# Kernel tuning notes

Measured on AMD Instinct MI355X. Metric: run time of the kernel, lower is better.

## Reference

```python
import jax, jax.numpy as jnp
import numpy as np

BITS = 4
MASK = (1 << BITS) - 1  # 15
PACK = 32 // BITS       # 8 values per int32


def setup_inputs() -> dict:
    key = jax.random.key(0)
    k1, k2, k3, k4, k5 = jax.random.split(key, 5)
    K, N, T = 4096, 4096, 8192
    x = jax.random.normal(k1, (T, K), dtype=jnp.float32)
    qweight = jax.random.randint(k2, (K * BITS // 32, N), 0, 2**31 - 1, dtype=jnp.int32)
    qzeros = jax.random.randint(k3, (1, N * BITS // 32), 0, 2**31 - 1, dtype=jnp.int32)
    scales = jax.random.uniform(k4, (1, N), dtype=jnp.float32) * 0.01
    g_idx = jnp.zeros((K,), dtype=jnp.int32)  # single group (group_size == infeatures)
    bias = jax.random.normal(k5, (N,), dtype=jnp.float32)
    return {"x": x, "qweight": qweight, "qzeros": qzeros, "scales": scales,
            "g_idx": g_idx, "bias": bias}


def reference(x, qweight, qzeros, scales, g_idx, bias):
    shifts = jnp.arange(0, 32, BITS, dtype=jnp.int32)  # (8,)
    # Unpack weights: (K/8, N) int32 -> (K/8, 8, N) -> (K, N) ints in [0, 15]
    w_int = (qweight[:, None, :] >> shifts[None, :, None]) & MASK
    K = w_int.shape[0] * PACK
    w_int = w_int.reshape(K, -1)
    # Unpack zero-points: (G, N/8) int32 -> (G, N/8, 8) -> (G, N), +1 per GPTQ convention
    z_int = ((qzeros[:, :, None] >> shifts[None, None, :]) & MASK) + 1
    z_int = z_int.reshape(scales.shape)  # (G, N)
    # Dequantize per input row via group index gather
    g = g_idx.astype(jnp.int32)
    w = scales[g] * (w_int.astype(scales.dtype) - z_int[g].astype(scales.dtype))  # (K, N)
    out = jnp.matmul(x, w) + bias  # (T, N)
    return out
```

## Files before the change

### kernel.cpp

```cpp
#include <hip/hip_runtime.h>
#include <stdint.h>

#define T_DIM 8192
#define K_DIM 4096
#define N_DIM 4096

typedef __attribute__((ext_vector_type(8))) short bf16x8;
typedef __attribute__((ext_vector_type(8))) unsigned short u16x8;
typedef __attribute__((ext_vector_type(4))) float f32x4;

__device__ __forceinline__ unsigned short f2bf(float f) {
  union { float f; uint32_t u; } c; c.f = f;
  uint32_t u = c.u;
  uint32_t r = (u + 0x7fffu + ((u >> 16) & 1u)) >> 16;
  return (unsigned short)r;
}
__device__ __forceinline__ float bf2f(unsigned short b) {
  union { uint32_t u; float f; } c; c.u = ((uint32_t)b) << 16;
  return c.f;
}

__global__ void unpack_bt(const int* __restrict__ qweight, const int* __restrict__ qzeros,
                          unsigned short* __restrict__ bt) {
  const int t  = threadIdx.x;
  const int n  = blockIdx.y * 32 + (t >> 3);
  const int kk = blockIdx.x * 8 + (t & 7);
  const int qw = qweight[(size_t)kk * N_DIM + n];
  const int zw = qzeros[n >> 3];
  const int z  = ((zw >> ((n & 7) * 4)) & 15) + 1;
  u16x8 v;
#pragma unroll
  for (int i = 0; i < 8; ++i) {
    const int w = (qw >> (4 * i)) & 15;
    v[i] = f2bf((float)(w - z));
  }
  *reinterpret_cast<u16x8*>(bt + (size_t)n * K_DIM + kk * 8) = v;
}

__global__ void split_x(const float* __restrict__ x, unsigned short* __restrict__ xhi,
                        unsigned short* __restrict__ xlo, int n8) {
  const int stride = gridDim.x * blockDim.x;
  for (int i = blockIdx.x * blockDim.x + threadIdx.x; i < n8; i += stride) {
    const float4 v0 = reinterpret_cast<const float4*>(x)[2 * i + 0];
    const float4 v1 = reinterpret_cast<const float4*>(x)[2 * i + 1];
    const float f[8] = {v0.x, v0.y, v0.z, v0.w, v1.x, v1.y, v1.z, v1.w};
    u16x8 h, l;
#pragma unroll
    for (int j = 0; j < 8; ++j) {
      const unsigned short hb = f2bf(f[j]);
      h[j] = hb;
      l[j] = f2bf(f[j] - bf2f(hb));
    }
    reinterpret_cast<u16x8*>(xhi)[i] = h;
    reinterpret_cast<u16x8*>(xlo)[i] = l;
  }
}

#define BM 128
#define BN 128
#define BK 32
#define NT (K_DIM / BK)
#define LDS_BUF 24576

__device__ __forceinline__ void gll16(const unsigned short* g, void* l) {
  __builtin_amdgcn_global_load_lds(
      (const __attribute__((address_space(1))) unsigned int*)g,
      (__attribute__((address_space(3))) unsigned int*)l, 16, 0, 0);
}

__global__ __launch_bounds__(256, 3) void gemm_dual(
    const unsigned short* __restrict__ xhi, const unsigned short* __restrict__ xlo,
    const unsigned short* __restrict__ bt, const float* __restrict__ scales,
    const float* __restrict__ bias, float* __restrict__ out) {
  __shared__ char lds[2 * LDS_BUF];
  const int tid  = threadIdx.x;
  const int lane = tid & 63;
  const int wid  = tid >> 6;

  const int bid = blockIdx.x;
  const int wg  = (bid & 7) * 256 + (bid >> 3);
  const int bx  = wg & 31;
  const int by  = wg >> 5;
  const int row0 = by * BM;
  const int col0 = bx * BN;

  const int r16 = lane & 15;
  const int kc  = lane >> 4;
  const int fA  = wid * 2;

  const unsigned short* sA0 = xhi + (size_t)(row0 + (fA + 0) * 16 + r16) * K_DIM + kc * 8;
  const unsigned short* sA1 = xhi + (size_t)(row0 + (fA + 1) * 16 + r16) * K_DIM + kc * 8;
  const unsigned short* sL0 = xlo + (size_t)(row0 + (fA + 0) * 16 + r16) * K_DIM + kc * 8;
  const unsigned short* sL1 = xlo + (size_t)(row0 + (fA + 1) * 16 + r16) * K_DIM + kc * 8;
  const unsigned short* sB0 = bt  + (size_t)(col0 + (fA + 0) * 16 + r16) * K_DIM + kc * 8;
  const unsigned short* sB1 = bt  + (size_t)(col0 + (fA + 1) * 16 + r16) * K_DIM + kc * 8;

  f32x4 acc[4][4];
#pragma unroll
  for (int i = 0; i < 4; ++i)
#pragma unroll
    for (int j = 0; j < 4; ++j) acc[i][j] = (f32x4){0.f, 0.f, 0.f, 0.f};

  const int wr = wid >> 1;
  const int wc = wid & 1;

  auto stage = [&](int buf, int t) {
    char* base   = lds + buf * LDS_BUF;
    const int ko = t * BK;
    gll16(sA0 + ko, base +         (fA + 0) * 1024);
    gll16(sA1 + ko, base +         (fA + 1) * 1024);
    gll16(sL0 + ko, base +  8192 + (fA + 0) * 1024);
    gll16(sL1 + ko, base +  8192 + (fA + 1) * 1024);
    gll16(sB0 + ko, base + 16384 + (fA + 0) * 1024);
    gll16(sB1 + ko, base + 16384 + (fA + 1) * 1024);
  };

  stage(0, 0);
  asm volatile("s_waitcnt vmcnt(0)" ::: "memory");
  __builtin_amdgcn_s_barrier();

  int cur = 0;
  for (int t = 0; t < NT; ++t) {
    if (t + 1 < NT) stage(cur ^ 1, t + 1);
    char* base = lds + cur * LDS_BUF;
    bf16x8 bf[4];
#pragma unroll
    for (int j = 0; j < 4; ++j)
      bf[j] = *reinterpret_cast<const bf16x8*>(base + 16384 + (wc * 4 + j) * 1024 + lane * 16);
#pragma unroll
    for (int i = 0; i < 4; ++i) {
      const bf16x8 ah = *reinterpret_cast<const bf16x8*>(base +        (wr * 4 + i) * 1024 + lane * 16);
      const bf16x8 al = *reinterpret_cast<const bf16x8*>(base + 8192 + (wr * 4 + i) * 1024 + lane * 16);
#pragma unroll
      for (int j = 0; j < 4; ++j)
        acc[i][j] = __builtin_amdgcn_mfma_f32_16x16x32_bf16(ah, bf[j], acc[i][j], 0, 0, 0);
#pragma unroll
      for (int j = 0; j < 4; ++j)
        acc[i][j] = __builtin_amdgcn_mfma_f32_16x16x32_bf16(al, bf[j], acc[i][j], 0, 0, 0);
    }
    asm volatile("s_waitcnt vmcnt(0)" ::: "memory");
    __builtin_amdgcn_s_barrier();
    cur ^= 1;
  }

#pragma unroll
  for (int j = 0; j < 4; ++j) {
    const int col = col0 + wc * 64 + j * 16 + r16;
    const float s = scales[col];
    const float b = bias[col];
#pragma unroll
    for (int i = 0; i < 4; ++i) {
      const int row = row0 + wr * 64 + i * 16 + kc * 4;
#pragma unroll
      for (int r = 0; r < 4; ++r) {
        out[(size_t)(row + r) * N_DIM + col] = s * acc[i][j][r] + b;
      }
    }
  }
}

extern "C" void kernel_launch(void* const* d_in, const int* in_sizes, int n_in,
                              void* d_out, int out_size, void* d_ws, size_t ws_size,
                              hipStream_t stream) {
  const float* x       = (const float*)d_in[0];
  const int*   qweight = (const int*)d_in[1];
  const int*   qzeros  = (const int*)d_in[2];
  const float* scales  = (const float*)d_in[3];
  const float* bias    = (const float*)d_in[5];
  float* out = (float*)d_out;

  char* ws = (char*)d_ws;
  unsigned short* bt  = (unsigned short*)ws;
  unsigned short* xhi = (unsigned short*)(ws + (size_t)32 * 1024 * 1024);
  unsigned short* xlo = (unsigned short*)(ws + (size_t)96 * 1024 * 1024);

  unpack_bt<<<dim3(K_DIM / 64, N_DIM / 32), 256, 0, stream>>>(qweight, qzeros, bt);
  split_x<<<dim3(4096), 256, 0, stream>>>(x, xhi, xlo, T_DIM * K_DIM / 8);
  gemm_dual<<<dim3((T_DIM / BM) * (N_DIM / BN)), 256, 0, stream>>>(xhi, xlo, bt, scales, bias, out);
}
```

Baseline: 972.2 us.

## Enlarge GEMM tile to 128x256x64 with 8 waves and interleaved prefetch

Moves the dual-bf16 GEMM from 4-wave 128x128x32 tiles to 8-wave 128x256x64 tiles with 128 KB of double-buffered LDS. The next tile's global-to-LDS loads are spread across the MFMA phases, with per-phase barriers and s_setprio raised around the MFMA groups. The aim is more operand reuse per byte loaded and better overlap of memory with matrix math. The cost is a per-phase barrier count several times higher and lower occupancy from the large LDS footprint.

```diff
diff --git a/kernel.cpp b/kernel.cpp
--- a/kernel.cpp
+++ b/kernel.cpp
@@ -57,10 +57,10 @@
 }
 
 #define BM 128
-#define BN 128
-#define BK 32
+#define BN 256
+#define BK 64
 #define NT (K_DIM / BK)
-#define LDS_BUF 24576
+#define BUF 65536
 
 __device__ __forceinline__ void gll16(const unsigned short* g, void* l) {
   __builtin_amdgcn_global_load_lds(
@@ -68,32 +68,32 @@
       (__attribute__((address_space(3))) unsigned int*)l, 16, 0, 0);
 }
 
-__global__ __launch_bounds__(256, 3) void gemm_dual(
+#define MFMA(a, b, c) __builtin_amdgcn_mfma_f32_16x16x32_bf16(a, b, c, 0, 0, 0)
+
+__global__ __launch_bounds__(512, 2) void gemm_dual8(
     const unsigned short* __restrict__ xhi, const unsigned short* __restrict__ xlo,
     const unsigned short* __restrict__ bt, const float* __restrict__ scales,
     const float* __restrict__ bias, float* __restrict__ out) {
-  __shared__ char lds[2 * LDS_BUF];
+  __shared__ char lds[2 * BUF];
   const int tid  = threadIdx.x;
   const int lane = tid & 63;
-  const int wid  = tid >> 6;
+  const int w    = tid >> 6;
+  const int wr   = w >> 2;
+  const int wc   = w & 3;
+  const int r16  = lane & 15;
+  const int kc   = lane >> 4;
 
   const int bid = blockIdx.x;
-  const int wg  = (bid & 7) * 256 + (bid >> 3);
-  const int bx  = wg & 31;
-  const int by  = wg >> 5;
+  const int wg  = (bid & 7) * 128 + (bid >> 3);
+  const int bx  = wg & 15;
+  const int by  = wg >> 4;
   const int row0 = by * BM;
   const int col0 = bx * BN;
 
-  const int r16 = lane & 15;
-  const int kc  = lane >> 4;
-  const int fA  = wid * 2;
-
-  const unsigned short* sA0 = xhi + (size_t)(row0 + (fA + 0) * 16 + r16) * K_DIM + kc * 8;
-  const unsigned short* sA1 = xhi + (size_t)(row0 + (fA + 1) * 16 + r16) * K_DIM + kc * 8;
-  const unsigned short* sL0 = xlo + (size_t)(row0 + (fA + 0) * 16 + r16) * K_DIM + kc * 8;
-  const unsigned short* sL1 = xlo + (size_t)(row0 + (fA + 1) * 16 + r16) * K_DIM + kc * 8;
-  const unsigned short* sB0 = bt  + (size_t)(col0 + (fA + 0) * 16 + r16) * K_DIM + kc * 8;
-  const unsigned short* sB1 = bt  + (size_t)(col0 + (fA + 1) * 16 + r16) * K_DIM + kc * 8;
+  const unsigned short* pA  = xhi + (size_t)(row0 + w * 16 + r16) * K_DIM + kc * 8;
+  const unsigned short* pL  = xlo + (size_t)(row0 + w * 16 + r16) * K_DIM + kc * 8;
+  const unsigned short* pB0 = bt  + (size_t)(col0 + (2 * w) * 16 + r16) * K_DIM + kc * 8;
+  const unsigned short* pB2 = pB0 + (size_t)16 * K_DIM;
 
   f32x4 acc[4][4];
 #pragma unroll
@@ -101,45 +101,66 @@
 #pragma unroll
     for (int j = 0; j < 4; ++j) acc[i][j] = (f32x4){0.f, 0.f, 0.f, 0.f};
 
-  const int wr = wid >> 1;
-  const int wc = wid & 1;
-
-  auto stage = [&](int buf, int t) {
-    char* base   = lds + buf * LDS_BUF;
-    const int ko = t * BK;
-    gll16(sA0 + ko, base +         (fA + 0) * 1024);
-    gll16(sA1 + ko, base +         (fA + 1) * 1024);
-    gll16(sL0 + ko, base +  8192 + (fA + 0) * 1024);
-    gll16(sL1 + ko, base +  8192 + (fA + 1) * 1024);
-    gll16(sB0 + ko, base + 16384 + (fA + 0) * 1024);
-    gll16(sB1 + ko, base + 16384 + (fA + 1) * 1024);
-  };
-
-  stage(0, 0);
+  {
+    char* b0 = lds;
+    gll16(pA,       b0 + (2 * w + 0) * 1024);
+    gll16(pA  + 32, b0 + (2 * w + 1) * 1024);
+    gll16(pL,       b0 + 16384 + (2 * w + 0) * 1024);
+    gll16(pL  + 32, b0 + 16384 + (2 * w + 1) * 1024);
+    gll16(pB0,      b0 + 32768 + (4 * w + 0) * 1024);
+    gll16(pB0 + 32, b0 + 32768 + (4 * w + 1) * 1024);
+    gll16(pB2,      b0 + 32768 + (4 * w + 2) * 1024);
+    gll16(pB2 + 32, b0 + 32768 + (4 * w + 3) * 1024);
+  }
   asm volatile("s_waitcnt vmcnt(0)" ::: "memory");
   __builtin_amdgcn_s_barrier();
 
   int cur = 0;
   for (int t = 0; t < NT; ++t) {
-    if (t + 1 < NT) stage(cur ^ 1, t + 1);
-    char* base = lds + cur * LDS_BUF;
-    bf16x8 bf[4];
-#pragma unroll
-    for (int j = 0; j < 4; ++j)
-      bf[j] = *reinterpret_cast<const bf16x8*>(base + 16384 + (wc * 4 + j) * 1024 + lane * 16);
-#pragma unroll
-    for (int i = 0; i < 4; ++i) {
-      const bf16x8 ah = *reinterpret_cast<const bf16x8*>(base +        (wr * 4 + i) * 1024 + lane * 16);
-      const bf16x8 al = *reinterpret_cast<const bf16x8*>(base + 8192 + (wr * 4 + i) * 1024 + lane * 16);
-#pragma unroll
-      for (int j = 0; j < 4; ++j)
-        acc[i][j] = __builtin_amdgcn_mfma_f32_16x16x32_bf16(ah, bf[j], acc[i][j], 0, 0, 0);
-#pragma unroll
-      for (int j = 0; j < 4; ++j)
-        acc[i][j] = __builtin_amdgcn_mfma_f32_16x16x32_bf16(al, bf[j], acc[i][j], 0, 0, 0);
+    const char* rb = lds + cur * BUF;
+    char* nb = lds + (cur ^ 1) * BUF;
+    const int koff = (t + 1) * BK;
+    const bool pf = (t + 1 < NT);
+#pragma unroll
+    for (int kh = 0; kh < 2; ++kh) {
+      bf16x8 bq0, bq1, bq2, bq3;
+#pragma unroll
+      for (int i = 0; i < 4; ++i) {
+        const int p = kh * 4 + i;
+        if (i == 0) {
+          bq0 = *reinterpret_cast<const bf16x8*>(rb + 32768 + ((wc * 4 + 0) * 2 + kh) * 1024 + lane * 16);
+          bq1 = *reinterpret_cast<const bf16x8*>(rb + 32768 + ((wc * 4 + 1) * 2 + kh) * 1024 + lane * 16);
+          bq2 = *reinterpret_cast<const bf16x8*>(rb + 32768 + ((wc * 4 + 2) * 2 + kh) * 1024 + lane * 16);
+          bq3 = *reinterpret_cast<const bf16x8*>(rb + 32768 + ((wc * 4 + 3) * 2 + kh) * 1024 + lane * 16);
+        }
+        const bf16x8 ah = *reinterpret_cast<const bf16x8*>(rb +         ((wr * 4 + i) * 2 + kh) * 1024 + lane * 16);
+        const bf16x8 al = *reinterpret_cast<const bf16x8*>(rb + 16384 + ((wr * 4 + i) * 2 + kh) * 1024 + lane * 16);
+        if (pf) {
+          if (p == 0) { gll16(pA  + koff, nb + (2 * w + 0) * 1024);
+                        gll16(pA  + koff + 32, nb + (2 * w + 1) * 1024); }
+          if (p == 1) { gll16(pL  + koff, nb + 16384 + (2 * w + 0) * 1024);
+                        gll16(pL  + koff + 32, nb + 16384 + (2 * w + 1) * 1024); }
+          if (p == 2) { gll16(pB0 + koff, nb + 32768 + (4 * w + 0) * 1024);
+                        gll16(pB0 + koff + 32, nb + 32768 + (4 * w + 1) * 1024); }
+          if (p == 3) { gll16(pB2 + koff, nb + 32768 + (4 * w + 2) * 1024);
+                        gll16(pB2 + koff + 32, nb + 32768 + (4 * w + 3) * 1024); }
+        }
+        __builtin_amdgcn_s_barrier();
+        asm volatile("s_waitcnt lgkmcnt(0)" ::: "memory");
+        __builtin_amdgcn_s_setprio(1);
+        acc[i][0] = MFMA(ah, bq0, acc[i][0]);
+        acc[i][1] = MFMA(ah, bq1, acc[i][1]);
+        acc[i][2] = MFMA(ah, bq2, acc[i][2]);
+        acc[i][3] = MFMA(ah, bq3, acc[i][3]);
+        acc[i][0] = MFMA(al, bq0, acc[i][0]);
+        acc[i][1] = MFMA(al, bq1, acc[i][1]);
+        acc[i][2] = MFMA(al, bq2, acc[i][2]);
+        acc[i][3] = MFMA(al, bq3, acc[i][3]);
+        __builtin_amdgcn_s_setprio(0);
+        if (p == 7) asm volatile("s_waitcnt vmcnt(0)" ::: "memory");
+        __builtin_amdgcn_s_barrier();
+      }
     }
-    asm volatile("s_waitcnt vmcnt(0)" ::: "memory");
-    __builtin_amdgcn_s_barrier();
     cur ^= 1;
   }
 
@@ -176,5 +197,5 @@
 
   unpack_bt<<<dim3(K_DIM / 64, N_DIM / 32), 256, 0, stream>>>(qweight, qzeros, bt);
   split_x<<<dim3(4096), 256, 0, stream>>>(x, xhi, xlo, T_DIM * K_DIM / 8);
-  gemm_dual<<<dim3((T_DIM / BM) * (N_DIM / BN)), 256, 0, stream>>>(xhi, xlo, bt, scales, bias, out);
-}
+  gemm_dual8<<<dim3((T_DIM / BM) * (N_DIM / BN)), 512, 0, stream>>>(xhi, xlo, bt, scales, bias, out);
+}
```

Result: faster. 875.7 us (-9.9%).
